# Performance work log

Measured on AMD Instinct MI355X. Metric: run time of the kernel, lower is better.

## Reference

```python
import jax, jax.numpy as jnp
import numpy as np

B, T, N, D, F, ORDER = 16, 12, 1024, 64, 64, 2
EPS = 1e-5  # BatchNorm eps (eval mode, running stats)


def setup_inputs() -> dict:
    key = jax.random.key(0)
    ks = jax.random.split(key, 8)
    C_eff = (ORDER + 1) * D  # (order*support_len + 1) * c_in = 192
    return {
        "x": jax.random.normal(ks[0], (B, T, N, D), jnp.float32),
        "A": jax.random.uniform(ks[1], (B, N, N), jnp.float32),  # dynamic per-sample adjacency
        "conv_w": jax.random.normal(ks[2], (F, C_eff), jnp.float32) / np.float32(np.sqrt(C_eff)),
        "conv_b": jnp.zeros((F,), jnp.float32),
        "bn_gamma": jnp.ones((F,), jnp.float32),
        "bn_beta": jnp.zeros((F,), jnp.float32),
        "bn_mean": 0.1 * jax.random.normal(ks[3], (F,), jnp.float32),
        "bn_var": jax.random.uniform(ks[4], (F,), jnp.float32) + 0.5,
        "gru_ff_w": jax.random.normal(ks[5], (T, 2 * F, 2 * F), jnp.float32) / np.float32(np.sqrt(2 * F)),
        "gru_ff_b": jnp.zeros((T, 2 * F), jnp.float32),
        "gru_zff_w": jax.random.normal(ks[6], (T, 2 * F, F), jnp.float32) / np.float32(np.sqrt(2 * F)),
        "gru_zff_b": jnp.zeros((T, F), jnp.float32),
    }


def _forward(x, A, conv_w, conv_b, bn_gamma, bn_beta, bn_mean, bn_var,
             gru_ff_w, gru_ff_b, gru_zff_w, gru_zff_b):
    # ---- DiffusionGraphEncoder ----
    xt = jnp.transpose(x, (0, 3, 2, 1))  # (B, C, N, T), matches torch transpose(1,3)
    outs = [xt]
    cur = xt
    for _ in range(ORDER):  # nconv: einsum('ncvl,nwv->ncwl')
        cur = jnp.einsum('bcvt,bwv->bcwt', cur, A)
        outs.append(cur)
    h = jnp.concatenate(outs, axis=1)        # (B, 3C, N, T)
    h = jnp.transpose(h, (0, 3, 2, 1))       # (B, T, N, C_eff)
    # ---- MLP1x1: 1x1 conv + eval-mode BatchNorm + relu ----
    y = jnp.einsum('btnc,fc->btnf', h, conv_w) + conv_b
    y = (y - bn_mean) * jax.lax.rsqrt(bn_var + EPS) * bn_gamma + bn_beta
    y = jax.nn.relu(y)  # dropout is identity at inference
    # ---- GRUEncoder: distinct GRUCellLite per timestep ----
    xs = jnp.transpose(y, (1, 0, 2, 3))      # (T, B, N, F)
    h0 = jnp.zeros((B, N, F), y.dtype)

    def step(hprev, inp):
        xt_, wff, bff, wzff, bzff = inp
        ru = jax.nn.sigmoid(jnp.concatenate([xt_, hprev], -1) @ wff + bff)
        r, u = ru[..., :F], ru[..., F:]
        z = jnp.tanh(jnp.concatenate([xt_, r * hprev], -1) @ wzff + bzff)
        hn = u * z + (1.0 - u) * hprev
        return hn, hn

    _, hs = jax.lax.scan(step, h0, (xs, gru_ff_w, gru_ff_b, gru_zff_w, gru_zff_b))
    return jnp.transpose(hs, (1, 0, 2, 3))   # (B, T, N, F)


def reference(x, A, conv_w, conv_b, bn_gamma, bn_beta, bn_mean, bn_var,
              gru_ff_w, gru_ff_b, gru_zff_w, gru_zff_b):
    return _forward(x, A, conv_w, conv_b, bn_gamma, bn_beta, bn_mean, bn_var,
                    gru_ff_w, gru_ff_b, gru_zff_w, gru_zff_b)
```

## Files before the change

kernel.cpp:

```cpp
#include <hip/hip_runtime.h>
#include <cstdint>
#include <cstddef>

#define NB 16
#define TT 12
#define NN 1024
#define DD 64
#define FF 64
#define JT 768

typedef __attribute__((ext_vector_type(8))) short v8s;
typedef __attribute__((ext_vector_type(4))) short v4s;
typedef __attribute__((ext_vector_type(4))) float v4f;

__device__ __forceinline__ float sigmoidf_(float v) { return 1.0f / (1.0f + expf(-v)); }

__device__ __forceinline__ float bf2f(unsigned short h) {
    union { unsigned int u; float f; } x; x.u = ((unsigned int)h) << 16; return x.f;
}
__device__ __forceinline__ unsigned short f2bf(float f) {
    union { float f; unsigned int u; } x; x.f = f;
    return (unsigned short)((x.u + 0x7fffu + ((x.u >> 16) & 1u)) >> 16);
}

__device__ __forceinline__ void gload16(const void* g, void* lds) {
    __builtin_amdgcn_global_load_lds(
        (const __attribute__((address_space(1))) void*)g,
        (__attribute__((address_space(3))) void*)lds, 16, 0, 0);
}

__global__ __launch_bounds__(256) void split_A(
    const float* __restrict__ A, unsigned short* __restrict__ Ah,
    unsigned short* __restrict__ Al)
{
    const size_t i0 = ((size_t)blockIdx.x * 256 + threadIdx.x) * 16;
    float v[16];
#pragma unroll
    for (int s = 0; s < 4; ++s)
        *(float4*)&v[s * 4] = *(const float4*)&A[i0 + s * 4];
    v8s h0, h1, l0, l1;
#pragma unroll
    for (int q = 0; q < 8; ++q) {
        unsigned short h = f2bf(v[q]);
        h0[q] = (short)h; l0[q] = (short)f2bf(v[q] - bf2f(h));
    }
#pragma unroll
    for (int q = 0; q < 8; ++q) {
        unsigned short h = f2bf(v[8 + q]);
        h1[q] = (short)h; l1[q] = (short)f2bf(v[8 + q] - bf2f(h));
    }
    *(v8s*)&Ah[i0] = h0; *(v8s*)&Ah[i0 + 8] = h1;
    *(v8s*)&Al[i0] = l0; *(v8s*)&Al[i0 + 8] = l1;
}

__global__ __launch_bounds__(256) void xsplitT(
    const float* __restrict__ x, unsigned short* __restrict__ Th,
    unsigned short* __restrict__ Tl)
{
    __shared__ float tile[64][68];
    const int v0 = blockIdx.x * 64, t = blockIdx.y, b = blockIdx.z;
    const int tid = threadIdx.x;
    {
        const int r = tid >> 2, q = (tid & 3) * 16;
#pragma unroll
        for (int s = 0; s < 4; ++s) {
            const float4 w = *(const float4*)&x[(((size_t)b * TT + t) * NN + v0 + r) * DD + q + s * 4];
            tile[r][q + s * 4 + 0] = w.x; tile[r][q + s * 4 + 1] = w.y;
            tile[r][q + s * 4 + 2] = w.z; tile[r][q + s * 4 + 3] = w.w;
        }
    }
    __syncthreads();
    {
        const int d = tid >> 2, vc = (tid & 3) * 16;
        const size_t base = ((size_t)b * JT + t * 64 + d) * 1024 + v0 + vc;
        v8s h0, h1, l0, l1;
#pragma unroll
        for (int s = 0; s < 8; ++s) {
            const float f = tile[vc + s][d];
            unsigned short h = f2bf(f);
            h0[s] = (short)h; l0[s] = (short)f2bf(f - bf2f(h));
        }
#pragma unroll
        for (int s = 0; s < 8; ++s) {
            const float f = tile[vc + 8 + s][d];
            unsigned short h = f2bf(f);
            h1[s] = (short)h; l1[s] = (short)f2bf(f - bf2f(h));
        }
        *(v8s*)&Th[base] = h0; *(v8s*)&Th[base + 8] = h1;
        *(v8s*)&Tl[base] = l0; *(v8s*)&Tl[base + 8] = l1;
    }
}

template<bool PAIROUT>
__global__ __launch_bounds__(256, 2) void gemm_bf(
    const unsigned short* __restrict__ Ah, const unsigned short* __restrict__ Al,
    const unsigned short* __restrict__ Bh, const unsigned short* __restrict__ Bl,
    unsigned short* __restrict__ Ch, unsigned short* __restrict__ Cl,
    float* __restrict__ Cf)
{
    __shared__ unsigned short LA[2][2][4096];
    __shared__ unsigned short LB[2][2][4096];

    const int wg = blockIdx.x;
    const int nlin = (wg & 7) * 96 + (wg >> 3);
    const int b  = nlin / 48;
    const int rr = nlin % 48;
    const int m0 = (rr / 6) * 128, n0 = (rr % 6) * 128;

    const int tid = threadIdx.x, lane = tid & 63, wid = tid >> 6;
    const int lr = lane & 15, hi = lane >> 4;
    const int wr = wid >> 1, wc = wid & 1;

    auto stage = [&](int buf, int kt) {
        const int rA = lane >> 2, kc = (lane & 3) * 8;
#pragma unroll
        for (int p = 0; p < 2; ++p) {
            const int c = wid * 2 + p;
            const size_t ga = ((size_t)b * 1024 + m0 + c * 16 + rA) * 1024 + kt * 32 + kc;
            gload16(Ah + ga, &LA[buf][0][c * 512]);
            gload16(Al + ga, &LA[buf][1][c * 512]);
            const size_t gb = ((size_t)b * JT + n0 + c * 16 + rA) * 1024 + kt * 32 + kc;
            gload16(Bh + gb, &LB[buf][0][c * 512]);
            gload16(Bl + gb, &LB[buf][1][c * 512]);
        }
    };

    v4f acc[4][4];
#pragma unroll
    for (int i = 0; i < 4; ++i)
#pragma unroll
        for (int j = 0; j < 4; ++j) acc[i][j] = (v4f){0.f, 0.f, 0.f, 0.f};

    stage(0, 0);
    __syncthreads();
    int cur = 0;
    for (int kt = 0; kt < 32; ++kt) {
        if (kt + 1 < 32) stage(cur ^ 1, kt + 1);
        v8s ah[4], al[4], bh[4], bl[4];
#pragma unroll
        for (int f = 0; f < 4; ++f) {
            const int m = wr * 64 + f * 16 + lr;
            ah[f] = *(const v8s*)&LA[cur][0][m * 32 + hi * 8];
            al[f] = *(const v8s*)&LA[cur][1][m * 32 + hi * 8];
        }
#pragma unroll
        for (int f = 0; f < 4; ++f) {
            const int n = wc * 64 + f * 16 + lr;
            bh[f] = *(const v8s*)&LB[cur][0][n * 32 + hi * 8];
            bl[f] = *(const v8s*)&LB[cur][1][n * 32 + hi * 8];
        }
#pragma unroll
        for (int fi = 0; fi < 4; ++fi)
#pragma unroll
            for (int fj = 0; fj < 4; ++fj) {
                acc[fi][fj] = __builtin_amdgcn_mfma_f32_16x16x32_bf16(ah[fi], bh[fj], acc[fi][fj], 0, 0, 0);
                acc[fi][fj] = __builtin_amdgcn_mfma_f32_16x16x32_bf16(ah[fi], bl[fj], acc[fi][fj], 0, 0, 0);
                acc[fi][fj] = __builtin_amdgcn_mfma_f32_16x16x32_bf16(al[fi], bh[fj], acc[fi][fj], 0, 0, 0);
            }
        __syncthreads();
        cur ^= 1;
    }

#pragma unroll
    for (int fi = 0; fi < 4; ++fi)
#pragma unroll
        for (int fj = 0; fj < 4; ++fj) {
            const int n  = n0 + wc * 64 + fj * 16 + lr;
            const int mb = m0 + wr * 64 + fi * 16 + hi * 4;
            const size_t o = ((size_t)b * JT + n) * 1024 + mb;
            if (PAIROUT) {
                v4s vh, vl;
#pragma unroll
                for (int r = 0; r < 4; ++r) {
                    const float v = acc[fi][fj][r];
                    const unsigned short h = f2bf(v);
                    vh[r] = (short)h; vl[r] = (short)f2bf(v - bf2f(h));
                }
                *(v4s*)&Ch[o] = vh;
                *(v4s*)&Cl[o] = vl;
            } else {
                float4 v = {acc[fi][fj][0], acc[fi][fj][1], acc[fi][fj][2], acc[fi][fj][3]};
                *(float4*)&Cf[o] = v;
            }
        }
}

template<bool XFROMX>
__global__ __launch_bounds__(256, 4) void gemm_f32(
    const float* __restrict__ Aop, const float* __restrict__ Xin,
    float* __restrict__ Xout)
{
    __shared__ float As[2][16 * 132];
    __shared__ float Bs[2][16 * 128];
    const int wg  = blockIdx.x;
    const int nlin = (wg & 7) * 96 + (wg >> 3);
    const int b  = nlin / 48;
    const int rr = nlin % 48;
    const int rb = rr / 6, cb = rr % 6;
    const int w0 = rb * 128, j0 = cb * 128;
    const int tid = threadIdx.x;
    const int rg = tid >> 4, cg = tid & 15;
    const int row0 = rg * 8;

    auto stage = [&](int buf, int kt) {
        const float* Ab = Aop + (size_t)b * NN * NN;
#pragma unroll
        for (int p = 0; p < 2; ++p) {
            const int c  = tid + p * 256;
            const int w  = c >> 2;
            const int k4 = (c & 3) * 4;
            const float4 v = *(const float4*)&Ab[(size_t)(w0 + w) * NN + kt * 16 + k4];
            As[buf][(k4 + 0) * 132 + w] = v.x;
            As[buf][(k4 + 1) * 132 + w] = v.y;
            As[buf][(k4 + 2) * 132 + w] = v.z;
            As[buf][(k4 + 3) * 132 + w] = v.w;
        }
#pragma unroll
        for (int p = 0; p < 2; ++p) {
            const int c = tid + p * 256;
            const int k = c >> 5;
            const int j = (c & 31) * 4;
            float4 v;
            if (XFROMX) {
                const int t = cb * 2 + (j >> 6);
                const int d = j & 63;
                v = *(const float4*)&Xin[(((size_t)b * TT + t) * NN + (size_t)kt * 16 + k) * DD + d];
            } else {
                v = *(const float4*)&Xin[((size_t)b * NN + (size_t)kt * 16 + k) * JT + j0 + j];
            }
            *(float4*)&Bs[buf][k * 128 + j] = v;
        }
    };

    float acc[8][8];
#pragma unroll
    for (int i = 0; i < 8; ++i)
#pragma unroll
        for (int j = 0; j < 8; ++j) acc[i][j] = 0.0f;

    stage(0, 0);
    __syncthreads();
    int cur = 0;
    for (int kt = 0; kt < 64; ++kt) {
        if (kt + 1 < 64) stage(cur ^ 1, kt + 1);
#pragma unroll
        for (int k = 0; k < 16; ++k) {
            float a[8], bb[8];
            *(float4*)&a[0]  = *(const float4*)&As[cur][k * 132 + row0];
            *(float4*)&a[4]  = *(const float4*)&As[cur][k * 132 + row0 + 4];
            *(float4*)&bb[0] = *(const float4*)&Bs[cur][k * 128 + cg * 4];
            *(float4*)&bb[4] = *(const float4*)&Bs[cur][k * 128 + 64 + cg * 4];
#pragma unroll
            for (int i = 0; i < 8; ++i)
#pragma unroll
                for (int j = 0; j < 8; ++j)
                    acc[i][j] = fmaf(a[i], bb[j], acc[i][j]);
        }
        __syncthreads();
        cur ^= 1;
    }
#pragma unroll
    for (int i = 0; i < 8; ++i) {
        float4 v0 = {acc[i][0], acc[i][1], acc[i][2], acc[i][3]};
        float4 v1 = {acc[i][4], acc[i][5], acc[i][6], acc[i][7]};
        float* dst = Xout + ((size_t)b * NN + w0 + row0 + i) * JT + j0;
        *(float4*)&dst[cg * 4]      = v0;
        *(float4*)&dst[64 + cg * 4] = v1;
    }
}

template<bool PAIRS>
__global__ __launch_bounds__(256) void conv_bn_relu(
    const float* __restrict__ x,
    const unsigned short* __restrict__ X1h, const unsigned short* __restrict__ X1l,
    const float* __restrict__ X2T,
    const float* __restrict__ X1f, const float* __restrict__ X2f,
    const float* __restrict__ W,
    const float* __restrict__ convb, const float* __restrict__ gamma,
    const float* __restrict__ beta,  const float* __restrict__ mean,
    const float* __restrict__ var,   float* __restrict__ y)
{
    __shared__ float As[64][132];
    __shared__ float Ws[64][68];
    const int nb = blockIdx.x, t = blockIdx.y, b = blockIdx.z;
    const int n0 = nb * 128;
    const int tid = threadIdx.x;
    const int rg = tid >> 4, cg = tid & 15;
    const int row0 = rg * 8, f0 = cg * 4;

    float acc[8][4];
#pragma unroll
    for (int i = 0; i < 8; ++i)
#pragma unroll
        for (int j = 0; j < 4; ++j) acc[i][j] = 0.0f;

    for (int kt = 0; kt < 3; ++kt) {
        __syncthreads();
        if (kt == 0) {
            const float* src = x + (((size_t)b * TT + t) * NN + n0) * DD;
#pragma unroll
            for (int p = 0; p < 8; ++p) {
                const int row = (tid >> 4) + p * 16;
                const int c4  = (tid & 15) * 4;
                const float4 v = *(const float4*)&src[(size_t)row * DD + c4];
                As[c4 + 0][row] = v.x; As[c4 + 1][row] = v.y;
                As[c4 + 2][row] = v.z; As[c4 + 3][row] = v.w;
            }
        } else if (PAIRS) {
            if (kt == 1) {
#pragma unroll
                for (int p = 0; p < 4; ++p) {
                    const int pos = p * 256 + tid;
                    const int c = pos >> 4, rw = (pos & 15) * 8;
                    const size_t o = ((size_t)b * JT + t * 64 + c) * 1024 + n0 + rw;
                    const v8s hv = *(const v8s*)&X1h[o];
                    const v8s lv = *(const v8s*)&X1l[o];
#pragma unroll
                    for (int q = 0; q < 8; ++q)
                        As[c][rw + q] = bf2f((unsigned short)hv[q]) + bf2f((unsigned short)lv[q]);
                }
            } else {
#pragma unroll
                for (int p = 0; p < 8; ++p) {
                    const int pos = p * 256 + tid;
                    const int c = pos >> 5, rw = (pos & 31) * 4;
                    const float4 v = *(const float4*)&X2T[((size_t)b * JT + t * 64 + c) * 1024 + n0 + rw];
                    As[c][rw + 0] = v.x; As[c][rw + 1] = v.y;
                    As[c][rw + 2] = v.z; As[c][rw + 3] = v.w;
                }
            }
        } else {
            const float* src = ((kt == 1) ? X1f : X2f) + ((size_t)b * NN + n0) * JT + t * DD;
#pragma unroll
            for (int p = 0; p < 8; ++p) {
                const int row = (tid >> 4) + p * 16;
                const int c4  = (tid & 15) * 4;
                const float4 v = *(const float4*)&src[(size_t)row * JT + c4];
                As[c4 + 0][row] = v.x; As[c4 + 1][row] = v.y;
                As[c4 + 2][row] = v.z; As[c4 + 3][row] = v.w;
            }
        }
#pragma unroll
        for (int p = 0; p < 4; ++p) {
            const int f  = (tid >> 4) + p * 16;
            const int c4 = (tid & 15) * 4;
            const float4 v = *(const float4*)&W[f * 192 + kt * 64 + c4];
            Ws[c4 + 0][f] = v.x; Ws[c4 + 1][f] = v.y;
            Ws[c4 + 2][f] = v.z; Ws[c4 + 3][f] = v.w;
        }
        __syncthreads();
#pragma unroll
        for (int k = 0; k < 64; ++k) {
            float a[8], w[4];
            *(float4*)&a[0] = *(const float4*)&As[k][row0];
            *(float4*)&a[4] = *(const float4*)&As[k][row0 + 4];
            *(float4*)&w[0] = *(const float4*)&Ws[k][f0];
#pragma unroll
            for (int i = 0; i < 8; ++i)
#pragma unroll
                for (int j = 0; j < 4; ++j)
                    acc[i][j] = fmaf(a[i], w[j], acc[i][j]);
        }
    }
    float s[4], off[4];
#pragma unroll
    for (int j = 0; j < 4; ++j) {
        const int f = f0 + j;
        const float sc = gamma[f] / sqrtf(var[f] + 1e-5f);
        s[j]   = sc;
        off[j] = (convb[f] - mean[f]) * sc + beta[f];
    }
#pragma unroll
    for (int i = 0; i < 8; ++i) {
        float4 v;
        v.x = fmaxf(acc[i][0] * s[0] + off[0], 0.0f);
        v.y = fmaxf(acc[i][1] * s[1] + off[1], 0.0f);
        v.z = fmaxf(acc[i][2] * s[2] + off[2], 0.0f);
        v.w = fmaxf(acc[i][3] * s[3] + off[3], 0.0f);
        *(float4*)&y[(((size_t)b * TT + t) * NN + n0 + row0 + i) * FF + f0] = v;
    }
}

__global__ __launch_bounds__(256) void gru_all(
    const float* __restrict__ y,    const float* __restrict__ wff,
    const float* __restrict__ bff,  const float* __restrict__ wzff,
    const float* __restrict__ bzff, float* __restrict__ out)
{
    __shared__ float Xs[64][36];
    __shared__ float Hs[64][36];
    __shared__ float Rs[64][36];
    __shared__ float Us[64][36];
    __shared__ float Ws[64][132];
    const int tid = threadIdx.x;
    const int mb  = blockIdx.x;
    const int b = mb >> 5, n0 = (mb & 31) * 32;
    const int rg = tid >> 5;
    const int og = tid & 31;

    for (int i = tid; i < 64 * 36; i += 256) (&Hs[0][0])[i] = 0.0f;

    for (int t = 0; t < TT; ++t) {
        {
            const float* xt = y + (((size_t)b * TT + t) * NN + n0) * DD;
            const int m = tid >> 3, c0 = (tid & 7) * 8;
            const float4 v0 = *(const float4*)&xt[m * DD + c0];
            const float4 v1 = *(const float4*)&xt[m * DD + c0 + 4];
            Xs[c0 + 0][m] = v0.x; Xs[c0 + 1][m] = v0.y;
            Xs[c0 + 2][m] = v0.z; Xs[c0 + 3][m] = v0.w;
            Xs[c0 + 4][m] = v1.x; Xs[c0 + 5][m] = v1.y;
            Xs[c0 + 6][m] = v1.z; Xs[c0 + 7][m] = v1.w;
        }
        float acc[4][4];
#pragma unroll
        for (int i = 0; i < 4; ++i)
#pragma unroll
            for (int j = 0; j < 4; ++j) acc[i][j] = 0.0f;

#pragma unroll
        for (int half = 0; half < 2; ++half) {
            __syncthreads();
#pragma unroll
            for (int p = 0; p < 8; ++p) {
                const int kk = (tid >> 5) + p * 8;
                const int o4 = (tid & 31) * 4;
                *(float4*)&Ws[kk][o4] =
                    *(const float4*)&wff[((size_t)t * 128 + half * 64 + kk) * 128 + o4];
            }
            __syncthreads();
            const float (*Asrc)[36] = half ? Hs : Xs;
#pragma unroll 4
            for (int kk = 0; kk < 64; ++kk) {
                const float4 av = *(const float4*)&Asrc[kk][rg * 4];
                const float4 wv = *(const float4*)&Ws[kk][og * 4];
                const float a0 = av.x, a1 = av.y, a2 = av.z, a3 = av.w;
                acc[0][0] = fmaf(a0, wv.x, acc[0][0]); acc[0][1] = fmaf(a0, wv.y, acc[0][1]);
                acc[0][2] = fmaf(a0, wv.z, acc[0][2]); acc[0][3] = fmaf(a0, wv.w, acc[0][3]);
                acc[1][0] = fmaf(a1, wv.x, acc[1][0]); acc[1][1] = fmaf(a1, wv.y, acc[1][1]);
                acc[1][2] = fmaf(a1, wv.z, acc[1][2]); acc[1][3] = fmaf(a1, wv.w, acc[1][3]);
                acc[2][0] = fmaf(a2, wv.x, acc[2][0]); acc[2][1] = fmaf(a2, wv.y, acc[2][1]);
                acc[2][2] = fmaf(a2, wv.z, acc[2][2]); acc[2][3] = fmaf(a2, wv.w, acc[2][3]);
                acc[3][0] = fmaf(a3, wv.x, acc[3][0]); acc[3][1] = fmaf(a3, wv.y, acc[3][1]);
                acc[3][2] = fmaf(a3, wv.z, acc[3][2]); acc[3][3] = fmaf(a3, wv.w, acc[3][3]);
            }
        }
        {
            const float4 bb4 = *(const float4*)&bff[(size_t)t * 128 + og * 4];
            float g[4][4];
#pragma unroll
            for (int i = 0; i < 4; ++i) {
                g[i][0] = sigmoidf_(acc[i][0] + bb4.x);
                g[i][1] = sigmoidf_(acc[i][1] + bb4.y);
                g[i][2] = sigmoidf_(acc[i][2] + bb4.z);
                g[i][3] = sigmoidf_(acc[i][3] + bb4.w);
            }
            if (og < 16) {
#pragma unroll
                for (int i = 0; i < 4; ++i)
#pragma unroll
                    for (int j = 0; j < 4; ++j) {
                        const int f = og * 4 + j, m = rg * 4 + i;
                        Rs[f][m] = g[i][j] * Hs[f][m];
                    }
            } else {
#pragma unroll
                for (int i = 0; i < 4; ++i)
#pragma unroll
                    for (int j = 0; j < 4; ++j)
                        Us[og * 4 + j - 64][rg * 4 + i] = g[i][j];
            }
        }
        float accz[4][2];
#pragma unroll
        for (int i = 0; i < 4; ++i) { accz[i][0] = 0.0f; accz[i][1] = 0.0f; }

#pragma unroll
        for (int half = 0; half < 2; ++half) {
            __syncthreads();
#pragma unroll
            for (int p = 0; p < 4; ++p) {
                const int kk = (tid >> 4) + p * 16;
                const int f4 = (tid & 15) * 4;
                *(float4*)&Ws[kk][f4] =
                    *(const float4*)&wzff[((size_t)t * 128 + half * 64 + kk) * 64 + f4];
            }
            __syncthreads();
            const float (*Asrc)[36] = half ? Rs : Xs;
#pragma unroll 4
            for (int kk = 0; kk < 64; ++kk) {
                const float4 av = *(const float4*)&Asrc[kk][rg * 4];
                const float2 wv = *(const float2*)&Ws[kk][og * 2];
                accz[0][0] = fmaf(av.x, wv.x, accz[0][0]); accz[0][1] = fmaf(av.x, wv.y, accz[0][1]);
                accz[1][0] = fmaf(av.y, wv.x, accz[1][0]); accz[1][1] = fmaf(av.y, wv.y, accz[1][1]);
                accz[2][0] = fmaf(av.z, wv.x, accz[2][0]); accz[2][1] = fmaf(av.z, wv.y, accz[2][1]);
                accz[3][0] = fmaf(av.w, wv.x, accz[3][0]); accz[3][1] = fmaf(av.w, wv.y, accz[3][1]);
            }
        }
        {
            const float2 bz = *(const float2*)&bzff[(size_t)t * 64 + og * 2];
            const int f0_ = og * 2;
#pragma unroll
            for (int i = 0; i < 4; ++i) {
                const int m = rg * 4 + i;
                const float z0 = tanhf(accz[i][0] + bz.x);
                const float z1 = tanhf(accz[i][1] + bz.y);
                const float u0 = Us[f0_][m],     u1 = Us[f0_ + 1][m];
                const float h0 = Hs[f0_][m],     h1 = Hs[f0_ + 1][m];
                const float hn0 = u0 * z0 + (1.0f - u0) * h0;
                const float hn1 = u1 * z1 + (1.0f - u1) * h1;
                Hs[f0_][m] = hn0; Hs[f0_ + 1][m] = hn1;
                *(float2*)&out[(((size_t)b * TT + t) * NN + n0 + m) * FF + f0_] =
                    make_float2(hn0, hn1);
            }
        }
        __syncthreads();
    }
}

extern "C" void kernel_launch(void* const* d_in, const int* in_sizes, int n_in,
                              void* d_out, int out_size, void* d_ws, size_t ws_size,
                              hipStream_t stream)
{
    const float* x        = (const float*)d_in[0];
    const float* A        = (const float*)d_in[1];
    const float* conv_w   = (const float*)d_in[2];
    const float* conv_b   = (const float*)d_in[3];
    const float* bn_gamma = (const float*)d_in[4];
    const float* bn_beta  = (const float*)d_in[5];
    const float* bn_mean  = (const float*)d_in[6];
    const float* bn_var   = (const float*)d_in[7];
    const float* gru_ff_w  = (const float*)d_in[8];
    const float* gru_ff_b  = (const float*)d_in[9];
    const float* gru_zff_w = (const float*)d_in[10];
    const float* gru_zff_b = (const float*)d_in[11];
    float* out = (float*)d_out;
    char* w = (char*)d_ws;

    const size_t szA_bf  = (size_t)NB * NN * NN * 2;
    const size_t szXT_bf = (size_t)NB * JT * NN * 2;
    const size_t needFast = 2 * szA_bf + 2 * szXT_bf + 2 * szXT_bf;

    dim3 gconv(8, TT, NB);

    if (ws_size >= needFast) {
        unsigned short* Ah2 = (unsigned short*)(w);
        unsigned short* Al2 = (unsigned short*)(w + szA_bf);
        unsigned short* X1h = (unsigned short*)(w + 2 * szA_bf);
        unsigned short* X1l = (unsigned short*)(w + 2 * szA_bf + szXT_bf);
        char* slot = w + 2 * szA_bf + 2 * szXT_bf;
        unsigned short* xh = (unsigned short*)slot;
        unsigned short* xl = (unsigned short*)(slot + szXT_bf);
        float* X2T = (float*)slot;
        float* yb  = (float*)w;

        xsplitT<<<dim3(16, TT, NB), 256, 0, stream>>>(x, xh, xl);
        split_A<<<4096, 256, 0, stream>>>(A, Ah2, Al2);
        gemm_bf<true ><<<768, 256, 0, stream>>>(Ah2, Al2, xh,  xl,  X1h, X1l, nullptr);
        gemm_bf<false><<<768, 256, 0, stream>>>(Ah2, Al2, X1h, X1l, nullptr, nullptr, X2T);
        conv_bn_relu<true><<<gconv, 256, 0, stream>>>(x, X1h, X1l, X2T, nullptr, nullptr,
                                                      conv_w, conv_b, bn_gamma, bn_beta,
                                                      bn_mean, bn_var, yb);
        gru_all<<<512, 256, 0, stream>>>(yb, gru_ff_w, gru_ff_b,
                                         gru_zff_w, gru_zff_b, out);
    } else {
        const size_t szX = (size_t)NB * NN * JT;
        float* X1 = (float*)w;
        float* X2 = X1 + szX;
        float* yb = X2 + szX;
        gemm_f32<true ><<<768, 256, 0, stream>>>(A, x,  X1);
        gemm_f32<false><<<768, 256, 0, stream>>>(A, X1, X2);
        conv_bn_relu<false><<<gconv, 256, 0, stream>>>(x, nullptr, nullptr, nullptr, X1, X2,
                                                       conv_w, conv_b, bn_gamma, bn_beta,
                                                       bn_mean, bn_var, yb);
        gru_all<<<512, 256, 0, stream>>>(yb, gru_ff_w, gru_ff_b,
                                         gru_zff_w, gru_zff_b, out);
    }
}
```

Measured before the change: 523.9 us.

## Move GRU recurrence onto bf16 MFMA with split-precision operands

Replaces the FP32 scalar GRU kernel with one that runs both GRU matmuls on bf16 MFMA. Inputs are split into three bf16 terms and hidden state into two, with weights pre-split by a new prep kernel into the workspace. Hidden state stays in swizzled shared memory across the timesteps. The graph GEMM also gains the low×low MFMA term for accuracy, which adds a quarter more MFMA work there. The split-precision scheme risks small accuracy loss and adds a launch plus workspace traffic for the weights.

```diff
diff --git a/kernel.cpp b/kernel.cpp
--- a/kernel.cpp
+++ b/kernel.cpp
@@ -156,6 +156,7 @@
                 acc[fi][fj] = __builtin_amdgcn_mfma_f32_16x16x32_bf16(ah[fi], bh[fj], acc[fi][fj], 0, 0, 0);
                 acc[fi][fj] = __builtin_amdgcn_mfma_f32_16x16x32_bf16(ah[fi], bl[fj], acc[fi][fj], 0, 0, 0);
                 acc[fi][fj] = __builtin_amdgcn_mfma_f32_16x16x32_bf16(al[fi], bh[fj], acc[fi][fj], 0, 0, 0);
+                acc[fi][fj] = __builtin_amdgcn_mfma_f32_16x16x32_bf16(al[fi], bl[fj], acc[fi][fj], 0, 0, 0);
             }
         __syncthreads();
         cur ^= 1;
@@ -381,6 +382,242 @@
     }
 }
 
+__global__ __launch_bounds__(256) void wprep3(
+    const float* __restrict__ wff, const float* __restrict__ wzff,
+    unsigned short* __restrict__ WF, unsigned short* __restrict__ WZ)
+{
+    const int t = blockIdx.x;
+    unsigned short* F = WF + (size_t)t * 40960;
+    for (int e = threadIdx.x; e < 8192; e += 256) {
+        const int o = e >> 6, k = e & 63;
+        const float vx = wff[((size_t)t * 128 + k) * 128 + o];
+        const unsigned short xh = f2bf(vx);
+        const float r1 = vx - bf2f(xh);
+        const unsigned short xm = f2bf(r1);
+        const unsigned short xl = f2bf(r1 - bf2f(xm));
+        F[0 * 8192 + o * 64 + k] = xh;
+        F[1 * 8192 + o * 64 + k] = xm;
+        F[2 * 8192 + o * 64 + k] = xl;
+        const float vh = wff[((size_t)t * 128 + 64 + k) * 128 + o];
+        const unsigned short hh = f2bf(vh);
+        const unsigned short hl = f2bf(vh - bf2f(hh));
+        F[3 * 8192 + o * 64 + k] = hh;
+        F[4 * 8192 + o * 64 + k] = hl;
+    }
+    unsigned short* Z = WZ + (size_t)t * 20480;
+    for (int e = threadIdx.x; e < 4096; e += 256) {
+        const int o = e >> 6, k = e & 63;
+        const float vx = wzff[((size_t)t * 128 + k) * 64 + o];
+        const unsigned short xh = f2bf(vx);
+        const float r1 = vx - bf2f(xh);
+        const unsigned short xm = f2bf(r1);
+        const unsigned short xl = f2bf(r1 - bf2f(xm));
+        Z[0 * 4096 + o * 64 + k] = xh;
+        Z[1 * 4096 + o * 64 + k] = xm;
+        Z[2 * 4096 + o * 64 + k] = xl;
+        const float vr = wzff[((size_t)t * 128 + 64 + k) * 64 + o];
+        const unsigned short rh = f2bf(vr);
+        const unsigned short rl = f2bf(vr - bf2f(rh));
+        Z[3 * 4096 + o * 64 + k] = rh;
+        Z[4 * 4096 + o * 64 + k] = rl;
+    }
+}
+
+__global__ __launch_bounds__(256, 2) void gru4(
+    const float* __restrict__ y,
+    const unsigned short* __restrict__ WF, const unsigned short* __restrict__ WZ,
+    const float* __restrict__ bff, const float* __restrict__ bzff,
+    float* __restrict__ out)
+{
+    __shared__ unsigned short Ahp[4096];
+    __shared__ unsigned short Rhp[4096];
+    __shared__ float Hs[32][68];
+
+    const int tid = threadIdx.x, lane = tid & 63, w = tid >> 6;
+    const int lr = lane & 15, hi = lane >> 4;
+    const int b = blockIdx.x >> 5, n0 = (blockIdx.x & 31) * 32;
+
+    for (int i = tid; i < 4096; i += 256) { Ahp[i] = 0; Rhp[i] = 0; }
+    for (int i = tid; i < 32 * 68; i += 256) (&Hs[0][0])[i] = 0.0f;
+    __syncthreads();
+
+    for (int t = 0; t < TT; ++t) {
+        v8s xa[2][2][3];
+        const float* yb = y + (((size_t)b * TT + t) * NN + n0) * 64;
+#pragma unroll
+        for (int mf = 0; mf < 2; ++mf)
+#pragma unroll
+            for (int kc = 0; kc < 2; ++kc) {
+                const int m = mf * 16 + lr;
+                float xv[8];
+                *(float4*)&xv[0] = *(const float4*)&yb[m * 64 + kc * 32 + hi * 8];
+                *(float4*)&xv[4] = *(const float4*)&yb[m * 64 + kc * 32 + hi * 8 + 4];
+                v8s h3, m3, l3;
+#pragma unroll
+                for (int q = 0; q < 8; ++q) {
+                    const float v = xv[q];
+                    const unsigned short hh = f2bf(v);
+                    const float r1 = v - bf2f(hh);
+                    const unsigned short mm = f2bf(r1);
+                    const unsigned short ll = f2bf(r1 - bf2f(mm));
+                    h3[q] = (short)hh; m3[q] = (short)mm; l3[q] = (short)ll;
+                }
+                xa[mf][kc][0] = h3; xa[mf][kc][1] = m3; xa[mf][kc][2] = l3;
+            }
+        v8s ha[2][2][2];
+#pragma unroll
+        for (int mf = 0; mf < 2; ++mf)
+#pragma unroll
+            for (int kc = 0; kc < 2; ++kc) {
+                const int m = mf * 16 + lr;
+                const int base = m * 128 + kc * 32 + hi * 8;
+                const int sw = (m & 7) << 3;
+                ha[mf][kc][0] = *(const v8s*)&Ahp[base ^ sw];
+                ha[mf][kc][1] = *(const v8s*)&Ahp[(base + 64) ^ sw];
+            }
+        __syncthreads();
+
+        v4f acc[2][2];
+#pragma unroll
+        for (int of = 0; of < 2; ++of)
+#pragma unroll
+            for (int mf = 0; mf < 2; ++mf) acc[of][mf] = (v4f){0.f, 0.f, 0.f, 0.f};
+
+#pragma unroll
+        for (int of = 0; of < 2; ++of) {
+            const int o = (2 * w + of) * 16 + lr;
+            v8s wx[2][3], wh_[2][2];
+#pragma unroll
+            for (int kc = 0; kc < 2; ++kc) {
+#pragma unroll
+                for (int lev = 0; lev < 3; ++lev)
+                    wx[kc][lev] = *(const v8s*)&WF[((size_t)t * 5 + lev) * 8192 + o * 64 + kc * 32 + hi * 8];
+#pragma unroll
+                for (int lev = 0; lev < 2; ++lev)
+                    wh_[kc][lev] = *(const v8s*)&WF[((size_t)t * 5 + 3 + lev) * 8192 + o * 64 + kc * 32 + hi * 8];
+            }
+#pragma unroll
+            for (int mf = 0; mf < 2; ++mf)
+#pragma unroll
+                for (int kc = 0; kc < 2; ++kc) {
+                    v4f a = acc[of][mf];
+                    a = __builtin_amdgcn_mfma_f32_16x16x32_bf16(xa[mf][kc][0], wx[kc][0], a, 0, 0, 0);
+                    a = __builtin_amdgcn_mfma_f32_16x16x32_bf16(xa[mf][kc][0], wx[kc][1], a, 0, 0, 0);
+                    a = __builtin_amdgcn_mfma_f32_16x16x32_bf16(xa[mf][kc][1], wx[kc][0], a, 0, 0, 0);
+                    a = __builtin_amdgcn_mfma_f32_16x16x32_bf16(xa[mf][kc][0], wx[kc][2], a, 0, 0, 0);
+                    a = __builtin_amdgcn_mfma_f32_16x16x32_bf16(xa[mf][kc][1], wx[kc][1], a, 0, 0, 0);
+                    a = __builtin_amdgcn_mfma_f32_16x16x32_bf16(xa[mf][kc][2], wx[kc][0], a, 0, 0, 0);
+                    a = __builtin_amdgcn_mfma_f32_16x16x32_bf16(ha[mf][kc][0], wh_[kc][0], a, 0, 0, 0);
+                    a = __builtin_amdgcn_mfma_f32_16x16x32_bf16(ha[mf][kc][0], wh_[kc][1], a, 0, 0, 0);
+                    a = __builtin_amdgcn_mfma_f32_16x16x32_bf16(ha[mf][kc][1], wh_[kc][0], a, 0, 0, 0);
+                    acc[of][mf] = a;
+                }
+        }
+        __syncthreads();
+
+        float u_[2][2][4];
+#pragma unroll
+        for (int of = 0; of < 2; ++of) {
+            const int o = (2 * w + of) * 16 + lr;
+            const float bv = bff[(size_t)t * 128 + o];
+#pragma unroll
+            for (int mf = 0; mf < 2; ++mf)
+#pragma unroll
+                for (int q = 0; q < 4; ++q) {
+                    const float g = sigmoidf_(acc[of][mf][q] + bv);
+                    if (w < 2) {
+                        const int m = mf * 16 + hi * 4 + q;
+                        const float rh = g * Hs[m][o];
+                        const unsigned short h = f2bf(rh);
+                        const unsigned short l = f2bf(rh - bf2f(h));
+                        const int sw = (m & 7) << 3;
+                        Rhp[(m * 128 + o) ^ sw]      = h;
+                        Rhp[(m * 128 + 64 + o) ^ sw] = l;
+                    } else {
+                        u_[of][mf][q] = g;
+                    }
+                }
+        }
+        __syncthreads();
+
+        v8s ra[2][2][2];
+#pragma unroll
+        for (int mf = 0; mf < 2; ++mf)
+#pragma unroll
+            for (int kc = 0; kc < 2; ++kc) {
+                const int m = mf * 16 + lr;
+                const int base = m * 128 + kc * 32 + hi * 8;
+                const int sw = (m & 7) << 3;
+                ra[mf][kc][0] = *(const v8s*)&Rhp[base ^ sw];
+                ra[mf][kc][1] = *(const v8s*)&Rhp[(base + 64) ^ sw];
+            }
+        __syncthreads();
+
+        v4f accz[2][2];
+#pragma unroll
+        for (int of = 0; of < 2; ++of)
+#pragma unroll
+            for (int mf = 0; mf < 2; ++mf) accz[of][mf] = (v4f){0.f, 0.f, 0.f, 0.f};
+
+#pragma unroll
+        for (int of = 0; of < 2; ++of) {
+            const int o = (w & 1) * 32 + of * 16 + lr;
+            v8s wx[2][3], wr_[2][2];
+#pragma unroll
+            for (int kc = 0; kc < 2; ++kc) {
+#pragma unroll
+                for (int lev = 0; lev < 3; ++lev)
+                    wx[kc][lev] = *(const v8s*)&WZ[((size_t)t * 5 + lev) * 4096 + o * 64 + kc * 32 + hi * 8];
+#pragma unroll
+                for (int lev = 0; lev < 2; ++lev)
+                    wr_[kc][lev] = *(const v8s*)&WZ[((size_t)t * 5 + 3 + lev) * 4096 + o * 64 + kc * 32 + hi * 8];
+            }
+#pragma unroll
+            for (int mf = 0; mf < 2; ++mf)
+#pragma unroll
+                for (int kc = 0; kc < 2; ++kc) {
+                    v4f a = accz[of][mf];
+                    a = __builtin_amdgcn_mfma_f32_16x16x32_bf16(xa[mf][kc][0], wx[kc][0], a, 0, 0, 0);
+                    a = __builtin_amdgcn_mfma_f32_16x16x32_bf16(xa[mf][kc][0], wx[kc][1], a, 0, 0, 0);
+                    a = __builtin_amdgcn_mfma_f32_16x16x32_bf16(xa[mf][kc][1], wx[kc][0], a, 0, 0, 0);
+                    a = __builtin_amdgcn_mfma_f32_16x16x32_bf16(xa[mf][kc][0], wx[kc][2], a, 0, 0, 0);
+                    a = __builtin_amdgcn_mfma_f32_16x16x32_bf16(xa[mf][kc][1], wx[kc][1], a, 0, 0, 0);
+                    a = __builtin_amdgcn_mfma_f32_16x16x32_bf16(xa[mf][kc][2], wx[kc][0], a, 0, 0, 0);
+                    a = __builtin_amdgcn_mfma_f32_16x16x32_bf16(ra[mf][kc][0], wr_[kc][0], a, 0, 0, 0);
+                    a = __builtin_amdgcn_mfma_f32_16x16x32_bf16(ra[mf][kc][0], wr_[kc][1], a, 0, 0, 0);
+                    a = __builtin_amdgcn_mfma_f32_16x16x32_bf16(ra[mf][kc][1], wr_[kc][0], a, 0, 0, 0);
+                    accz[of][mf] = a;
+                }
+        }
+        __syncthreads();
+
+        if (w >= 2) {
+#pragma unroll
+            for (int of = 0; of < 2; ++of) {
+                const int o = (w & 1) * 32 + of * 16 + lr;
+                const float bz = bzff[(size_t)t * 64 + o];
+#pragma unroll
+                for (int mf = 0; mf < 2; ++mf)
+#pragma unroll
+                    for (int q = 0; q < 4; ++q) {
+                        const int m = mf * 16 + hi * 4 + q;
+                        const float z = tanhf(accz[of][mf][q] + bz);
+                        const float u = u_[of][mf][q];
+                        const float hn = u * z + (1.0f - u) * Hs[m][o];
+                        Hs[m][o] = hn;
+                        const unsigned short h = f2bf(hn);
+                        const unsigned short l = f2bf(hn - bf2f(h));
+                        const int sw = (m & 7) << 3;
+                        Ahp[(m * 128 + o) ^ sw]      = h;
+                        Ahp[(m * 128 + 64 + o) ^ sw] = l;
+                        out[(((size_t)b * TT + t) * NN + n0 + m) * 64 + o] = hn;
+                    }
+            }
+        }
+        __syncthreads();
+    }
+}
+
 __global__ __launch_bounds__(256) void gru_all(
     const float* __restrict__ y,    const float* __restrict__ wff,
     const float* __restrict__ bff,  const float* __restrict__ wzff,
@@ -550,7 +787,9 @@
         unsigned short* xh = (unsigned short*)slot;
         unsigned short* xl = (unsigned short*)(slot + szXT_bf);
         float* X2T = (float*)slot;
-        float* yb  = (float*)w;
+        float* yb = (float*)w;
+        unsigned short* WF = (unsigned short*)(w + 50331648);
+        unsigned short* WZ = (unsigned short*)(w + 50331648 + 983040);
 
         xsplitT<<<dim3(16, TT, NB), 256, 0, stream>>>(x, xh, xl);
         split_A<<<4096, 256, 0, stream>>>(A, Ah2, Al2);
@@ -559,8 +798,8 @@
         conv_bn_relu<true><<<gconv, 256, 0, stream>>>(x, X1h, X1l, X2T, nullptr, nullptr,
                                                       conv_w, conv_b, bn_gamma, bn_beta,
                                                       bn_mean, bn_var, yb);
-        gru_all<<<512, 256, 0, stream>>>(yb, gru_ff_w, gru_ff_b,
-                                         gru_zff_w, gru_zff_b, out);
+        wprep3<<<TT, 256, 0, stream>>>(gru_ff_w, gru_zff_w, WF, WZ);
+        gru4<<<512, 256, 0, stream>>>(yb, WF, WZ, gru_ff_b, gru_zff_b, out);
     } else {
         const size_t szX = (size_t)NB * NN * JT;
         float* X1 = (float*)w;
```

Measured after the change: 543.5 us. 3.7% more time.
